# Performance work log

Measured on AMD Instinct MI355X. Metric: run time of the kernel, lower is better.

Reference implementation:

```python
import math
import jax, jax.numpy as jnp
import numpy as np

LMAX = 6
SH_DIM = (LMAX + 1) ** 2
NUM_INV = LMAX + 1
SILU_SCALE = 1.0 / 0.6  # ScaledSiLU


def scaled_silu(x):
    return jax.nn.silu(x) * SILU_SCALE


def sph_harm(v):
    """Real spherical harmonics up to LMAX, 'component' normalization, input normalized. [*, 3] -> [*, SH_DIM]."""
    n = jnp.sqrt(jnp.sum(v * v, axis=-1, keepdims=True) + 1e-12)
    v = v / n
    x, y, z = v[..., 0], v[..., 1], v[..., 2]
    st = jnp.sqrt(jnp.clip(x * x + y * y, 0.0, None))  # sin(theta)
    phi = jnp.arctan2(y, x)
    # fully-normalized associated Legendre P[(l,m)] via standard recurrences
    P = {(0, 0): jnp.full_like(z, math.sqrt(1.0 / (4.0 * math.pi)))}
    for m in range(1, LMAX + 1):
        P[(m, m)] = -math.sqrt((2 * m + 1) / (2.0 * m)) * st * P[(m - 1, m - 1)]
    for m in range(0, LMAX):
        P[(m + 1, m)] = math.sqrt(2 * m + 3) * z * P[(m, m)]
    for m in range(0, LMAX + 1):
        for l in range(m + 2, LMAX + 1):
            a = math.sqrt((4 * l * l - 1.0) / (l * l - m * m))
            b = math.sqrt(((l - 1) ** 2 - m * m) / (4.0 * (l - 1) ** 2 - 1.0))
            P[(l, m)] = a * (z * P[(l - 1, m)] - b * P[(l - 2, m)])
    s4pi = math.sqrt(4.0 * math.pi)
    sq2 = math.sqrt(2.0)
    cols = []
    for l in range(LMAX + 1):
        for m in range(-l, l + 1):
            if m < 0:
                cols.append(s4pi * sq2 * P[(l, -m)] * jnp.sin(-m * phi))
            elif m == 0:
                cols.append(s4pi * P[(l, 0)])
            else:
                cols.append(s4pi * sq2 * P[(l, m)] * jnp.cos(m * phi))
    return jnp.stack(cols, axis=-1)


def sh_bilinear_inv(sh1, sh2):
    """Per-l mean of elementwise product. [E, SH_DIM] x2 -> [E, NUM_INV]."""
    outs, idx = [], 0
    for l in range(LMAX + 1):
        d = 2 * l + 1
        outs.append(jnp.mean(sh1[:, idx:idx + d] * sh2[:, idx:idx + d], axis=-1))
        idx += d
    return jnp.stack(outs, axis=-1)


def _forward(node_scalar, node_vector, edge_rbf, edge_udiff, edge_index,
             W_edge, b_edge, W_x1, b_x1, W_x2, b_x2, ln_g, ln_b, W_inv, b_inv):
    H = node_scalar.shape[1]
    N = node_scalar.shape[0]
    j, i = edge_index[0], edge_index[1]
    inv_sqrt3 = 1.0 / math.sqrt(3.0)
    inv_sqrt_h = 1.0 / math.sqrt(H)

    rbf_h = edge_rbf @ W_edge + b_edge  # [E, 3H]

    # scatter-mean of edge directions onto receiving nodes
    counts = jax.ops.segment_sum(jnp.ones_like(i, dtype=edge_udiff.dtype), i, num_segments=N)
    ref_vec = jax.ops.segment_sum(edge_udiff, i, num_segments=N) / jnp.maximum(counts, 1.0)[:, None]
    ref_norm = jnp.sqrt(jnp.sum(ref_vec * ref_vec, axis=-1, keepdims=True) + 1e-9)
    ref_vec = ref_vec / ref_norm
    zero_mask = ref_norm[:, 0] < 5e-5
    default_vec = jnp.array([1.0, 0.0, 0.0], dtype=ref_vec.dtype)
    ref_vec = jnp.where(zero_mask[:, None], default_vec, ref_vec)

    edge_sh = sph_harm(edge_udiff)          # [E, SH_DIM]
    ref_sh = sph_harm(ref_vec)[i]           # [E, SH_DIM]
    inv = sh_bilinear_inv(edge_sh, ref_sh)  # [E, NUM_INV]
    mu = jnp.mean(inv, axis=-1, keepdims=True)
    var = jnp.var(inv, axis=-1, keepdims=True)
    inv = (inv - mu) / jnp.sqrt(var + 1e-5) * ln_g + ln_b

    cos_theta = jnp.sum(edge_udiff * ref_vec[i], axis=-1, keepdims=True)  # [E,1]
    geom = jnp.concatenate([cos_theta, inv], axis=-1)  # [E, NUM_INV+1]
    gate = jnp.tanh(scaled_silu(geom @ W_inv + b_inv))
    rbf_h = rbf_h * (1.0 + gate)

    scalar_proj = scaled_silu(node_scalar @ W_x1 + b_x1) @ W_x2 + b_x2  # [N, 3H]
    x_ji = scalar_proj[j] * rbf_h * inv_sqrt3
    x1, x2, x3 = x_ji[:, :H], x_ji[:, H:2 * H], x_ji[:, 2 * H:]

    vec_ji = (x1[:, None, :] * node_vector[j] + x2[:, None, :] * edge_udiff[:, :, None]) * inv_sqrt_h  # [E,3,H]
    delta_vector = jax.ops.segment_sum(vec_ji, i, num_segments=N)
    delta_scalar = jax.ops.segment_sum(x3, i, num_segments=N)
    return delta_scalar, delta_vector


def setup_inputs() -> dict:
    N, E, H, R = 50000, 400000, 64, 64
    key = jax.random.key(0)
    ks = jax.random.split(key, 16)
    ud = jax.random.normal(ks[3], (E, 3), dtype=jnp.float32)
    ud = ud / jnp.linalg.norm(ud, axis=-1, keepdims=True)
    s = 0.05
    return {
        "node_scalar": jax.random.normal(ks[0], (N, H), dtype=jnp.float32),
        "node_vector": jax.random.normal(ks[1], (N, 3, H), dtype=jnp.float32),
        "edge_rbf": jax.random.uniform(ks[2], (E, R), dtype=jnp.float32),
        "edge_udiff": ud,
        "edge_index": jax.random.randint(ks[4], (2, E), 0, N, dtype=jnp.int32),
        "W_edge": jax.random.normal(ks[5], (R, 3 * H), dtype=jnp.float32) * s,
        "b_edge": jnp.zeros((3 * H,), dtype=jnp.float32),
        "W_x1": jax.random.normal(ks[6], (H, H // 2), dtype=jnp.float32) * s,
        "b_x1": jnp.zeros((H // 2,), dtype=jnp.float32),
        "W_x2": jax.random.normal(ks[7], (H // 2, 3 * H), dtype=jnp.float32) * s,
        "b_x2": jnp.zeros((3 * H,), dtype=jnp.float32),
        "ln_g": jnp.ones((NUM_INV,), dtype=jnp.float32),
        "ln_b": jnp.zeros((NUM_INV,), dtype=jnp.float32),
        "W_inv": jax.random.normal(ks[8], (NUM_INV + 1, 3 * H), dtype=jnp.float32) * s,
        "b_inv": jnp.zeros((3 * H,), dtype=jnp.float32),
    }


def reference(node_scalar, node_vector, edge_rbf, edge_udiff, edge_index,
              W_edge, b_edge, W_x1, b_x1, W_x2, b_x2, ln_g, ln_b, W_inv, b_inv):
    return _forward(node_scalar, node_vector, edge_rbf, edge_udiff, edge_index,
                    W_edge, b_edge, W_x1, b_x1, W_x2, b_x2, ln_g, ln_b, W_inv, b_inv)
```

## Files before the change

### kernel.cpp

```cpp
#include <hip/hip_runtime.h>
#include <math.h>

#define LMAXX 6
#define SH49 49
#define TPB 256
#define TILE_E 64
#define SCB 256
#define CAPS 14

typedef __attribute__((ext_vector_type(8))) short short8v;
typedef __attribute__((ext_vector_type(16))) float f32x16;
union FragU { short8v v; uint2 u2[2]; };

__device__ __forceinline__ unsigned pack_bf16(float a, float b) {
    unsigned ua = __float_as_uint(a);
    unsigned ub = __float_as_uint(b);
    ua += 0x7fffu + ((ua >> 16) & 1u);
    ub += 0x7fffu + ((ub >> 16) & 1u);
    return (ua >> 16) | (ub & 0xffff0000u);
}
__device__ __forceinline__ float bf16_lo(unsigned w) { return __uint_as_float(w << 16); }
__device__ __forceinline__ float bf16_hi(unsigned w) { return __uint_as_float(w & 0xffff0000u); }

__device__ __forceinline__ void sph49(float x, float y, float z, float* sh) {
    float nn = sqrtf(x * x + y * y + z * z + 1e-12f);
    float iv = 1.0f / nn;
    x *= iv; y *= iv; z *= iv;
    float st2 = x * x + y * y;
    float st = sqrtf(st2 > 0.f ? st2 : 0.f);
    float cphi, sphi;
    if (st > 1e-30f) { cphi = x / st; sphi = y / st; }
    else { cphi = 1.0f; sphi = 0.0f; }

    float P[LMAXX + 1][LMAXX + 1];
    P[0][0] = 0.28209479177387814f;
#pragma unroll
    for (int m = 1; m <= LMAXX; ++m)
        P[m][m] = -sqrtf((2.f * m + 1.f) / (2.f * m)) * st * P[m - 1][m - 1];
#pragma unroll
    for (int m = 0; m < LMAXX; ++m)
        P[m + 1][m] = sqrtf(2.f * m + 3.f) * z * P[m][m];
#pragma unroll
    for (int m = 0; m <= LMAXX; ++m) {
#pragma unroll
        for (int l = m + 2; l <= LMAXX; ++l) {
            float a = sqrtf((4.f * l * l - 1.f) / (float)(l * l - m * m));
            float b = sqrtf((float)((l - 1) * (l - 1) - m * m) /
                            (4.f * (l - 1) * (l - 1) - 1.f));
            P[l][m] = a * (z * P[l - 1][m] - b * P[l - 2][m]);
        }
    }
    float cm[LMAXX + 1], sm[LMAXX + 1];
    cm[0] = 1.f; sm[0] = 0.f; cm[1] = cphi; sm[1] = sphi;
#pragma unroll
    for (int m = 2; m <= LMAXX; ++m) {
        cm[m] = 2.f * cphi * cm[m - 1] - cm[m - 2];
        sm[m] = 2.f * cphi * sm[m - 1] - sm[m - 2];
    }
    const float s4pi = 3.5449077018110318f;
    const float s8pi = 5.0132565492620005f;
    int idx = 0;
#pragma unroll
    for (int l = 0; l <= LMAXX; ++l) {
#pragma unroll
        for (int mm = -l; mm <= l; ++mm) {
            if (mm < 0)       sh[idx++] = s8pi * P[l][-mm] * sm[-mm];
            else if (mm == 0) sh[idx++] = s4pi * P[l][0];
            else              sh[idx++] = s8pi * P[l][mm] * cm[mm];
        }
    }
}

__global__ void k_hist(const int* __restrict__ eidx, int* __restrict__ icnt, int E) {
    int e = blockIdx.x * blockDim.x + threadIdx.x;
    if (e >= E) return;
    atomicAdd(&icnt[eidx[E + e]], 1);
}

__global__ void k_scan1(const int* __restrict__ icnt, int* __restrict__ offs,
                        int* __restrict__ bsum, int N) {
    __shared__ int s[SCB];
    int t = threadIdx.x;
    int idx = blockIdx.x * SCB + t;
    int v = (idx < N) ? icnt[idx] : 0;
    s[t] = v; __syncthreads();
#pragma unroll
    for (int off = 1; off < SCB; off <<= 1) {
        int u = (t >= off) ? s[t - off] : 0;
        __syncthreads();
        s[t] += u;
        __syncthreads();
    }
    if (idx < N) offs[idx] = s[t] - v;
    if (t == SCB - 1) bsum[blockIdx.x] = s[t];
}

__global__ void k_scan2(int* __restrict__ bsum, int nb) {
    __shared__ int s[1024];
    int t = threadIdx.x;
    int v = (t < nb) ? bsum[t] : 0;
    s[t] = v; __syncthreads();
#pragma unroll
    for (int off = 1; off < 1024; off <<= 1) {
        int u = (t >= off) ? s[t - off] : 0;
        __syncthreads();
        s[t] += u;
        __syncthreads();
    }
    if (t < nb) bsum[t] = s[t] - v;
}

__global__ void k_scan3(int* __restrict__ offs, const int* __restrict__ bsum,
                        int* __restrict__ cursor, int N) {
    int idx = blockIdx.x * SCB + threadIdx.x;
    if (idx >= N) return;
    int o = offs[idx] + bsum[blockIdx.x];
    offs[idx] = o;
    cursor[idx] = o;
}

__global__ void k_perm(const float* __restrict__ ud, const int* __restrict__ eidx,
                       int* __restrict__ cursor, int* __restrict__ perm,
                       int* __restrict__ ii_s, int* __restrict__ jj_s,
                       float* __restrict__ ud_s, int E) {
    int e = blockIdx.x * blockDim.x + threadIdx.x;
    if (e >= E) return;
    int i = eidx[E + e];
    int j = eidx[e];
    int pos = atomicAdd(&cursor[i], 1);
    perm[pos] = e;
    ii_s[pos] = i;
    jj_s[pos] = j;
    ud_s[3 * pos + 0] = ud[3 * e + 0];
    ud_s[3 * pos + 1] = ud[3 * e + 1];
    ud_s[3 * pos + 2] = ud[3 * e + 2];
}

__global__ void k_node_ref(const int* __restrict__ offs, const int* __restrict__ icnt,
                           const float* __restrict__ ud_s,
                           float* __restrict__ ref_vec, float* __restrict__ ref_sh,
                           int N) {
    int n = blockIdx.x * blockDim.x + threadIdx.x;
    if (n >= N) return;
    int o0 = offs[n], c = icnt[n];
    float sx = 0.f, sy = 0.f, sz = 0.f;
    for (int e = o0; e < o0 + c; ++e) {
        sx += ud_s[3 * e + 0];
        sy += ud_s[3 * e + 1];
        sz += ud_s[3 * e + 2];
    }
    float d = fmaxf((float)c, 1.0f);
    float vx = sx / d, vy = sy / d, vz = sz / d;
    float norm = sqrtf(vx * vx + vy * vy + vz * vz + 1e-9f);
    float ivn = 1.0f / norm;
    vx *= ivn; vy *= ivn; vz *= ivn;
    if (norm < 5e-5f) { vx = 1.f; vy = 0.f; vz = 0.f; }
    ref_vec[3 * n + 0] = vx;
    ref_vec[3 * n + 1] = vy;
    ref_vec[3 * n + 2] = vz;
    sph49(vx, vy, vz, ref_sh + (size_t)n * SH49);
}

__global__ __launch_bounds__(TPB) void k_sproj(const float* __restrict__ ns,
                                               const float* __restrict__ W1,
                                               const float* __restrict__ b1,
                                               const float* __restrict__ W2,
                                               const float* __restrict__ b2,
                                               unsigned* __restrict__ spj_p, int N) {
    __shared__ float sW1[64 * 32];
    __shared__ float sW2[32 * 192];
    __shared__ float sb2[192];
    __shared__ float sb1[32];
    __shared__ float sbuf[4][64];
    __shared__ float h1buf[4][32];
    __shared__ float srow[4][192];
    int t = threadIdx.x;
    for (int p = t; p < 64 * 32; p += TPB) sW1[p] = W1[p];
    for (int p = t; p < 32 * 192; p += TPB) sW2[p] = W2[p];
    if (t < 192) sb2[t] = b2[t];
    if (t < 32) sb1[t] = b1[t];

    int w = t >> 6, l = t & 63;
    int nwaves = gridDim.x * 4;
    int iters = (N + nwaves - 1) / nwaves;
    for (int it = 0; it < iters; ++it) {
        int n = blockIdx.x * 4 + w + it * nwaves;
        bool act = n < N;
        __syncthreads();
        if (act) sbuf[w][l] = ns[(size_t)n * 64 + l];
        __syncthreads();
        if (act) {
            int k = l & 31;
            float h = sb1[k];
#pragma unroll
            for (int c = 0; c < 64; ++c) h = fmaf(sbuf[w][c], sW1[c * 32 + k], h);
            float sig = 1.0f / (1.0f + __expf(-h));
            h = h * sig * (1.0f / 0.6f);
            if (l < 32) h1buf[w][l] = h;
        }
        __syncthreads();
        if (act) {
#pragma unroll
            for (int m = 0; m < 3; ++m) {
                int o = l + 64 * m;
                float a = sb2[o];
#pragma unroll
                for (int kk = 0; kk < 32; ++kk)
                    a = fmaf(h1buf[w][kk], sW2[kk * 192 + o], a);
                srow[w][o] = a;
            }
        }
        __syncthreads();
        if (act) {
            {
                int ww = l;
                if (ww < 96) {
                    int oc = ww & 31, q = ww >> 5;
                    spj_p[(size_t)n * 96 + ww] =
                        pack_bf16(srow[w][64 * q + oc], srow[w][64 * q + oc + 32]);
                }
            }
            if (l < 32) {
                int ww = 64 + l;
                int oc = ww & 31, q = ww >> 5;
                spj_p[(size_t)n * 96 + ww] =
                    pack_bf16(srow[w][64 * q + oc], srow[w][64 * q + oc + 32]);
            }
        }
    }
}

__global__ void k_nvp(const float* __restrict__ nvec, unsigned* __restrict__ nvp,
                      int total ) {
    int idx = blockIdx.x * blockDim.x + threadIdx.x;
    if (idx >= total) return;
    int n = idx / 96, w = idx - n * 96;
    int d = w >> 5, oc = w & 31;
    size_t base = (size_t)n * 192 + d * 64 + oc;
    nvp[idx] = pack_bf16(nvec[base], nvec[base + 32]);
}

__global__ void k_geom_s(const float* __restrict__ ud_s, const int* __restrict__ ii_s,
                         const float* __restrict__ ref_vec,
                         const float* __restrict__ ref_sh,
                         const float* __restrict__ ln_g, const float* __restrict__ ln_b,
                         float* __restrict__ geom_s, int E) {
    int r = blockIdx.x * blockDim.x + threadIdx.x;
    if (r >= E) return;
    int i = ii_s[r];
    float ux = ud_s[3 * r], uy = ud_s[3 * r + 1], uz = ud_s[3 * r + 2];
    float esh[SH49];
    sph49(ux, uy, uz, esh);
    const float* rs = ref_sh + (size_t)i * SH49;
    float inv[7];
    int idx = 0;
#pragma unroll
    for (int l = 0; l <= 6; ++l) {
        float s = 0.f;
#pragma unroll
        for (int m = 0; m < 2 * l + 1; ++m) { s += esh[idx] * rs[idx]; idx++; }
        inv[l] = s / (float)(2 * l + 1);
    }
    float mu = 0.f;
#pragma unroll
    for (int l = 0; l < 7; ++l) mu += inv[l];
    mu *= (1.0f / 7.0f);
    float var = 0.f;
#pragma unroll
    for (int l = 0; l < 7; ++l) { float d = inv[l] - mu; var += d * d; }
    var *= (1.0f / 7.0f);
    float rstd = rsqrtf(var + 1e-5f);
    float rvx = ref_vec[3 * i], rvy = ref_vec[3 * i + 1], rvz = ref_vec[3 * i + 2];
    float ct = ux * rvx + uy * rvy + uz * rvz;
    float* g = geom_s + (size_t)r * 8;
    g[0] = ct;
#pragma unroll
    for (int l = 0; l < 7; ++l) g[1 + l] = (inv[l] - mu) * rstd * ln_g[l] + ln_b[l];
}

__global__ __launch_bounds__(TPB, 3) void k_main(
    const float* __restrict__ rbf, const float* __restrict__ W_edge,
    const float* __restrict__ b_edge, const float* __restrict__ W_inv,
    const float* __restrict__ b_inv, const float* __restrict__ geom_s,
    const unsigned* __restrict__ spj_p, const unsigned* __restrict__ nvp,
    const float* __restrict__ ud_s, const int* __restrict__ ii_s,
    const int* __restrict__ jj_s, const int* __restrict__ perm,
    float* __restrict__ dscal, float* __restrict__ dvec, int E) {
    __shared__ __align__(16) unsigned sWT[192 * 34];
    __shared__ __align__(16) unsigned rbfT[64 * 34];
    __shared__ __align__(16) float sgeom[64 * 8];
    __shared__ float sud[64 * 3];
    __shared__ int sii[64];
    __shared__ int sjj[64];
    __shared__ int sslot[64];
    __shared__ int sfirst[64];
    __shared__ int sD;
    __shared__ float sacc[CAPS * 256];

    int t = threadIdx.x;
    int l = t & 63;
    int wid = t >> 6;
    int eh = wid >> 1;
    int wc = wid & 1;
    int lo5 = l & 31;
    int hi = l >> 5;
    int h = wc * 32 + lo5;

    for (int p = t; p < 192 * 32; p += TPB) {
        int col = p >> 5, kd = p & 31;
        sWT[col * 34 + kd] = pack_bf16(W_edge[(2 * kd) * 192 + col],
                                       W_edge[(2 * kd + 1) * 192 + col]);
    }

    float wv_inv[8][3];
#pragma unroll
    for (int c = 0; c < 8; ++c)
#pragma unroll
        for (int q = 0; q < 3; ++q)
            wv_inv[c][q] = W_inv[c * 192 + q * 64 + h];
    float bi[3], be[3];
#pragma unroll
    for (int q = 0; q < 3; ++q) {
        bi[q] = b_inv[q * 64 + h];
        be[q] = b_edge[q * 64 + h];
    }

    const float inv_sqrt3 = 0.57735026918962584f;
    const float inv_sqrt_h = 0.125f;

    int ntiles = (E + TILE_E - 1) / TILE_E;
    for (int tile = blockIdx.x; tile < ntiles; tile += gridDim.x) {
        int e0 = tile * TILE_E;
        __syncthreads();
        if (t < 64) {
            int rg = e0 + t;
            sjj[t] = (rg < E) ? jj_s[rg] : 0;
            sii[t] = (rg < E) ? ii_s[rg] : -1;
        }
        for (int p = t; p < 64 * 8; p += TPB)
            sgeom[p] = (e0 + (p >> 3) < E) ? geom_s[(size_t)e0 * 8 + p] : 0.f;
        for (int p = t; p < 64 * 3; p += TPB)
            sud[p] = (e0 + p / 3 < E) ? ud_s[(size_t)e0 * 3 + p] : 0.f;
        {
            int e = t >> 2, q4 = t & 3;
            int rg = e0 + e;
            int dst = e * 34 + q4 * 8;
            if (rg < E) {
                const float4* src = (const float4*)&rbf[(size_t)perm[rg] * 64 + q4 * 16];
                float4 v0 = src[0], v1 = src[1], v2 = src[2], v3 = src[3];
                rbfT[dst + 0] = pack_bf16(v0.x, v0.y);
                rbfT[dst + 1] = pack_bf16(v0.z, v0.w);
                rbfT[dst + 2] = pack_bf16(v1.x, v1.y);
                rbfT[dst + 3] = pack_bf16(v1.z, v1.w);
                rbfT[dst + 4] = pack_bf16(v2.x, v2.y);
                rbfT[dst + 5] = pack_bf16(v2.z, v2.w);
                rbfT[dst + 6] = pack_bf16(v3.x, v3.y);
                rbfT[dst + 7] = pack_bf16(v3.z, v3.w);
            } else {
#pragma unroll
                for (int q = 0; q < 8; ++q) rbfT[dst + q] = 0u;
            }
        }
        __syncthreads();

        if (t < 64) {
            bool flag = (t == 0) || (sii[t] != sii[t - 1]);
            unsigned long long bal = __ballot(flag);
            unsigned long long mask =
                (t == 63) ? ~0ull : ((1ull << (t + 1)) - 1ull);
            int slot = __popcll(bal & mask) - 1;
            sslot[t] = slot;
            if (flag) sfirst[slot] = t;
            if (t == 0) sD = __popcll(bal);
        }

        FragU afr[4];
        int arow = lo5 + 32 * eh;
#pragma unroll
        for (int ks = 0; ks < 4; ++ks) {
            int off = arow * 34 + ks * 8 + hi * 4;
            afr[ks].u2[0] = *(const uint2*)&rbfT[off];
            afr[ks].u2[1] = *(const uint2*)&rbfT[off + 2];
        }
        f32x16 acc0 = {0.f,0.f,0.f,0.f,0.f,0.f,0.f,0.f,0.f,0.f,0.f,0.f,0.f,0.f,0.f,0.f};
        f32x16 acc1 = acc0, acc2 = acc0;
        int bc0 = (wc * 32 + lo5) * 34;
#pragma unroll
        for (int ks = 0; ks < 4; ++ks) {
            int off = ks * 8 + hi * 4;
            FragU b0, b1, b2;
            b0.u2[0] = *(const uint2*)&sWT[bc0 + off];
            b0.u2[1] = *(const uint2*)&sWT[bc0 + off + 2];
            b1.u2[0] = *(const uint2*)&sWT[bc0 + 64 * 34 + off];
            b1.u2[1] = *(const uint2*)&sWT[bc0 + 64 * 34 + off + 2];
            b2.u2[0] = *(const uint2*)&sWT[bc0 + 128 * 34 + off];
            b2.u2[1] = *(const uint2*)&sWT[bc0 + 128 * 34 + off + 2];
            acc0 = __builtin_amdgcn_mfma_f32_32x32x16_bf16(afr[ks].v, b0.v, acc0, 0, 0, 0);
            acc1 = __builtin_amdgcn_mfma_f32_32x32x16_bf16(afr[ks].v, b1.v, acc1, 0, 0, 0);
            acc2 = __builtin_amdgcn_mfma_f32_32x32x16_bf16(afr[ks].v, b2.v, acc2, 0, 0, 0);
        }

        __syncthreads();
        int D = sD;
        bool slotmode = (D <= CAPS);
        if (slotmode) {
            for (int p = t; p < D * 256; p += TPB) sacc[p] = 0.f;
        }
        __syncthreads();

        float a_s = 0.f, a_v0 = 0.f, a_v1 = 0.f, a_v2 = 0.f;
        int runi = -1, runslot = -1;
        auto flush = [&]() {
            if (runi < 0) return;
            if (slotmode) {
                float* sa = &sacc[runslot * 256];
                atomicAdd(&sa[h], a_s);
                atomicAdd(&sa[64 + h], a_v0);
                atomicAdd(&sa[128 + h], a_v1);
                atomicAdd(&sa[192 + h], a_v2);
            } else {
                atomicAdd(&dscal[(size_t)runi * 64 + h], a_s);
                atomicAdd(&dvec[(size_t)runi * 192 + h], a_v0);
                atomicAdd(&dvec[(size_t)runi * 192 + 64 + h], a_v1);
                atomicAdd(&dvec[(size_t)runi * 192 + 128 + h], a_v2);
            }
        };
#pragma unroll
        for (int r = 0; r < 16; ++r) {
            int el = eh * 32 + (r & 3) + 8 * (r >> 2) + 4 * hi;
            int rg = e0 + el;
            if (rg < E) {
                int i = sii[el], j = sjj[el];
                if (i != runi) {
                    flush();
                    a_s = 0.f; a_v0 = 0.f; a_v1 = 0.f; a_v2 = 0.f;
                    runi = i; runslot = sslot[el];
                }
                float4 g0 = *(const float4*)&sgeom[el * 8];
                float4 g1 = *(const float4*)&sgeom[el * 8 + 4];
                float u0 = bi[0], u1 = bi[1], u2 = bi[2];
                float gg[8] = {g0.x, g0.y, g0.z, g0.w, g1.x, g1.y, g1.z, g1.w};
#pragma unroll
                for (int c = 0; c < 8; ++c) {
                    u0 = fmaf(gg[c], wv_inv[c][0], u0);
                    u1 = fmaf(gg[c], wv_inv[c][1], u1);
                    u2 = fmaf(gg[c], wv_inv[c][2], u2);
                }
                float gate[3];
                float uu[3] = {u0, u1, u2};
#pragma unroll
                for (int q = 0; q < 3; ++q) {
                    float u = uu[q];
                    float sig = 1.0f / (1.0f + __expf(-u));
                    float v = u * sig * (1.0f / 0.6f);
                    v = fminf(fmaxf(v, -20.f), 20.f);
                    float e2v = __expf(2.0f * v);
                    gate[q] = (e2v - 1.0f) / (e2v + 1.0f);
                }
                size_t jb = (size_t)j * 96;
                unsigned spw0 = spj_p[jb + lo5];
                unsigned spw1 = spj_p[jb + 32 + lo5];
                unsigned spw2 = spj_p[jb + 64 + lo5];
                float sp0 = wc ? bf16_hi(spw0) : bf16_lo(spw0);
                float sp1 = wc ? bf16_hi(spw1) : bf16_lo(spw1);
                float sp2 = wc ? bf16_hi(spw2) : bf16_lo(spw2);
                float x1 = sp0 * (acc0[r] + be[0]) * (1.0f + gate[0]) * inv_sqrt3;
                float x2 = sp1 * (acc1[r] + be[1]) * (1.0f + gate[1]) * inv_sqrt3;
                float x3 = sp2 * (acc2[r] + be[2]) * (1.0f + gate[2]) * inv_sqrt3;
                a_s += x3;
                float ud0 = sud[el * 3], ud1 = sud[el * 3 + 1], ud2 = sud[el * 3 + 2];
                unsigned nw0 = nvp[jb + lo5];
                unsigned nw1 = nvp[jb + 32 + lo5];
                unsigned nw2 = nvp[jb + 64 + lo5];
                float nv0 = wc ? bf16_hi(nw0) : bf16_lo(nw0);
                float nv1 = wc ? bf16_hi(nw1) : bf16_lo(nw1);
                float nv2 = wc ? bf16_hi(nw2) : bf16_lo(nw2);
                a_v0 += (x1 * nv0 + x2 * ud0) * inv_sqrt_h;
                a_v1 += (x1 * nv1 + x2 * ud1) * inv_sqrt_h;
                a_v2 += (x1 * nv2 + x2 * ud2) * inv_sqrt_h;
            }
        }
        flush();
        __syncthreads();

        if (slotmode) {
            int Dreal = D - ((sii[63] < 0) ? 1 : 0);
            for (int s = 0; s < D; ++s) {
                int n = sii[sfirst[s]];
                if (n < 0) continue;
                float val = sacc[s * 256 + t];
                bool boundary = (s == 0) || (s == Dreal - 1);
                float* ptr = (t < 64) ? &dscal[(size_t)n * 64 + t]
                                      : &dvec[(size_t)n * 192 + (t - 64)];
                if (boundary) atomicAdd(ptr, val);
                else *ptr = val;
            }
        }
    }
}

extern "C" void kernel_launch(void* const* d_in, const int* in_sizes, int n_in,
                              void* d_out, int out_size, void* d_ws, size_t ws_size,
                              hipStream_t stream) {
    const float* node_scalar = (const float*)d_in[0];
    const float* node_vector = (const float*)d_in[1];
    const float* edge_rbf    = (const float*)d_in[2];
    const float* edge_udiff  = (const float*)d_in[3];
    const int*   edge_index  = (const int*)d_in[4];
    const float* W_edge      = (const float*)d_in[5];
    const float* b_edge      = (const float*)d_in[6];
    const float* W_x1        = (const float*)d_in[7];
    const float* b_x1        = (const float*)d_in[8];
    const float* W_x2        = (const float*)d_in[9];
    const float* b_x2        = (const float*)d_in[10];
    const float* ln_g        = (const float*)d_in[11];
    const float* ln_b        = (const float*)d_in[12];
    const float* W_inv       = (const float*)d_in[13];
    const float* b_inv       = (const float*)d_in[14];

    int N = in_sizes[0] / 64;
    int E = in_sizes[3] / 3;

    float* ws = (float*)d_ws;
    size_t o = 0;
    int*      icnt   = (int*)(ws + o); o += N;
    int*      offs   = (int*)(ws + o); o += N;
    int*      cursor = (int*)(ws + o); o += N;
    int*      bsum   = (int*)(ws + o); o += 1024;
    float*    ref_vec= ws + o; o += (size_t)N * 3;
    float*    ref_sh = ws + o; o += (size_t)N * SH49;
    unsigned* spj_p  = (unsigned*)(ws + o); o += (size_t)N * 96;
    unsigned* nvp    = (unsigned*)(ws + o); o += (size_t)N * 96;
    int*      perm   = (int*)(ws + o); o += E;
    float*    geom_s = ws + o; o += (size_t)E * 8;
    float*    ud_s   = ws + o; o += (size_t)E * 3;
    int*      ii_s   = (int*)(ws + o); o += E;
    int*      jj_s   = (int*)(ws + o); o += E;

    float* dscal = (float*)d_out;
    float* dvec  = (float*)d_out + (size_t)N * 64;

    hipMemsetAsync(icnt, 0, (size_t)N * sizeof(int), stream);
    hipMemsetAsync(d_out, 0, (size_t)out_size * sizeof(float), stream);

    int nb = (N + SCB - 1) / SCB;

    k_hist<<<(E + TPB - 1) / TPB, TPB, 0, stream>>>(edge_index, icnt, E);
    k_scan1<<<nb, SCB, 0, stream>>>(icnt, offs, bsum, N);
    k_scan2<<<1, 1024, 0, stream>>>(bsum, nb);
    k_scan3<<<nb, SCB, 0, stream>>>(offs, bsum, cursor, N);
    k_perm<<<(E + TPB - 1) / TPB, TPB, 0, stream>>>(edge_udiff, edge_index, cursor,
                                                    perm, ii_s, jj_s, ud_s, E);
    k_node_ref<<<(N + TPB - 1) / TPB, TPB, 0, stream>>>(offs, icnt, ud_s,
                                                        ref_vec, ref_sh, N);
    k_sproj<<<512, TPB, 0, stream>>>(node_scalar, W_x1, b_x1, W_x2, b_x2, spj_p, N);
    k_nvp<<<(N * 96 + TPB - 1) / TPB, TPB, 0, stream>>>(node_vector, nvp, N * 96);
    k_geom_s<<<(E + TPB - 1) / TPB, TPB, 0, stream>>>(ud_s, ii_s, ref_vec, ref_sh,
                                                      ln_g, ln_b, geom_s, E);
    k_main<<<768, TPB, 0, stream>>>(edge_rbf, W_edge, b_edge, W_inv, b_inv, geom_s,
                                    spj_p, nvp, ud_s, ii_s, jj_s, perm,
                                    dscal, dvec, E);
}
```

Measured before the change: 632.4 us.

## Fuse node gather buffers, compute SH invariant via Legendre product, drop LDS staging

Result: faster. 576.2 us (-8.9%).

```diff
diff --git a/kernel.cpp b/kernel.cpp
--- a/kernel.cpp
+++ b/kernel.cpp
@@ -2,11 +2,10 @@
 #include <math.h>
 
 #define LMAXX 6
-#define SH49 49
 #define TPB 256
 #define TILE_E 64
 #define SCB 256
-#define CAPS 14
+#define CAPS 12
 
 typedef __attribute__((ext_vector_type(8))) short short8v;
 typedef __attribute__((ext_vector_type(16))) float f32x16;
@@ -22,17 +21,18 @@
 __device__ __forceinline__ float bf16_lo(unsigned w) { return __uint_as_float(w << 16); }
 __device__ __forceinline__ float bf16_hi(unsigned w) { return __uint_as_float(w & 0xffff0000u); }
 
-__device__ __forceinline__ void sph49(float x, float y, float z, float* sh) {
+__device__ __forceinline__ void dirang(float x, float y, float z,
+                                       float& zo, float& st, float& cphi, float& sphi) {
     float nn = sqrtf(x * x + y * y + z * z + 1e-12f);
     float iv = 1.0f / nn;
-    x *= iv; y *= iv; z *= iv;
+    x *= iv; y *= iv; zo = z * iv;
     float st2 = x * x + y * y;
-    float st = sqrtf(st2 > 0.f ? st2 : 0.f);
-    float cphi, sphi;
+    st = sqrtf(st2 > 0.f ? st2 : 0.f);
     if (st > 1e-30f) { cphi = x / st; sphi = y / st; }
     else { cphi = 1.0f; sphi = 0.0f; }
-
-    float P[LMAXX + 1][LMAXX + 1];
+}
+
+__device__ __forceinline__ void legP(float z, float st, float P[7][7]) {
     P[0][0] = 0.28209479177387814f;
 #pragma unroll
     for (int m = 1; m <= LMAXX; ++m)
@@ -48,25 +48,6 @@
             float b = sqrtf((float)((l - 1) * (l - 1) - m * m) /
                             (4.f * (l - 1) * (l - 1) - 1.f));
             P[l][m] = a * (z * P[l - 1][m] - b * P[l - 2][m]);
-        }
-    }
-    float cm[LMAXX + 1], sm[LMAXX + 1];
-    cm[0] = 1.f; sm[0] = 0.f; cm[1] = cphi; sm[1] = sphi;
-#pragma unroll
-    for (int m = 2; m <= LMAXX; ++m) {
-        cm[m] = 2.f * cphi * cm[m - 1] - cm[m - 2];
-        sm[m] = 2.f * cphi * sm[m - 1] - sm[m - 2];
-    }
-    const float s4pi = 3.5449077018110318f;
-    const float s8pi = 5.0132565492620005f;
-    int idx = 0;
-#pragma unroll
-    for (int l = 0; l <= LMAXX; ++l) {
-#pragma unroll
-        for (int mm = -l; mm <= l; ++mm) {
-            if (mm < 0)       sh[idx++] = s8pi * P[l][-mm] * sm[-mm];
-            else if (mm == 0) sh[idx++] = s4pi * P[l][0];
-            else              sh[idx++] = s8pi * P[l][mm] * cm[mm];
         }
     }
 }
@@ -138,8 +119,7 @@
 
 __global__ void k_node_ref(const int* __restrict__ offs, const int* __restrict__ icnt,
                            const float* __restrict__ ud_s,
-                           float* __restrict__ ref_vec, float* __restrict__ ref_sh,
-                           int N) {
+                           float* __restrict__ ref_vec, int N) {
     int n = blockIdx.x * blockDim.x + threadIdx.x;
     if (n >= N) return;
     int o0 = offs[n], c = icnt[n];
@@ -158,22 +138,21 @@
     ref_vec[3 * n + 0] = vx;
     ref_vec[3 * n + 1] = vy;
     ref_vec[3 * n + 2] = vz;
-    sph49(vx, vy, vz, ref_sh + (size_t)n * SH49);
-}
-
-__global__ __launch_bounds__(TPB) void k_sproj(const float* __restrict__ ns,
-                                               const float* __restrict__ W1,
-                                               const float* __restrict__ b1,
-                                               const float* __restrict__ W2,
-                                               const float* __restrict__ b2,
-                                               unsigned* __restrict__ spj_p, int N) {
+}
+
+__global__ __launch_bounds__(TPB) void k_sprojv(const float* __restrict__ ns,
+                                                const float* __restrict__ W1,
+                                                const float* __restrict__ b1,
+                                                const float* __restrict__ W2,
+                                                const float* __restrict__ b2,
+                                                const float* __restrict__ nvec,
+                                                unsigned* __restrict__ gat, int N) {
     __shared__ float sW1[64 * 32];
     __shared__ float sW2[32 * 192];
     __shared__ float sb2[192];
     __shared__ float sb1[32];
     __shared__ float sbuf[4][64];
     __shared__ float h1buf[4][32];
-    __shared__ float srow[4][192];
     int t = threadIdx.x;
     for (int p = t; p < 64 * 32; p += TPB) sW1[p] = W1[p];
     for (int p = t; p < 32 * 192; p += TPB) sW2[p] = W2[p];
@@ -200,67 +179,70 @@
         }
         __syncthreads();
         if (act) {
+            float a[3];
 #pragma unroll
             for (int m = 0; m < 3; ++m) {
                 int o = l + 64 * m;
-                float a = sb2[o];
+                float acc = sb2[o];
 #pragma unroll
                 for (int kk = 0; kk < 32; ++kk)
-                    a = fmaf(h1buf[w][kk], sW2[kk * 192 + o], a);
-                srow[w][o] = a;
+                    acc = fmaf(h1buf[w][kk], sW2[kk * 192 + o], acc);
+                a[m] = acc;
             }
-        }
-        __syncthreads();
-        if (act) {
-            {
-                int ww = l;
-                if (ww < 96) {
-                    int oc = ww & 31, q = ww >> 5;
-                    spj_p[(size_t)n * 96 + ww] =
-                        pack_bf16(srow[w][64 * q + oc], srow[w][64 * q + oc + 32]);
-                }
-            }
-            if (l < 32) {
-                int ww = 64 + l;
-                int oc = ww & 31, q = ww >> 5;
-                spj_p[(size_t)n * 96 + ww] =
-                    pack_bf16(srow[w][64 * q + oc], srow[w][64 * q + oc + 32]);
-            }
-        }
-    }
-}
-
-__global__ void k_nvp(const float* __restrict__ nvec, unsigned* __restrict__ nvp,
-                      int total ) {
-    int idx = blockIdx.x * blockDim.x + threadIdx.x;
-    if (idx >= total) return;
-    int n = idx / 96, w = idx - n * 96;
-    int d = w >> 5, oc = w & 31;
-    size_t base = (size_t)n * 192 + d * 64 + oc;
-    nvp[idx] = pack_bf16(nvec[base], nvec[base + 32]);
+            size_t nb = (size_t)n * 192;
+            float nv0 = nvec[nb + l];
+            float nv1 = nvec[nb + 64 + l];
+            float nv2 = nvec[nb + 128 + l];
+            gat[nb + l]        = pack_bf16(a[0], a[1]);
+            gat[nb + 64 + l]   = pack_bf16(a[2], nv0);
+            gat[nb + 128 + l]  = pack_bf16(nv1, nv2);
+        }
+    }
 }
 
 __global__ void k_geom_s(const float* __restrict__ ud_s, const int* __restrict__ ii_s,
                          const float* __restrict__ ref_vec,
-                         const float* __restrict__ ref_sh,
                          const float* __restrict__ ln_g, const float* __restrict__ ln_b,
                          float* __restrict__ geom_s, int E) {
     int r = blockIdx.x * blockDim.x + threadIdx.x;
     if (r >= E) return;
     int i = ii_s[r];
     float ux = ud_s[3 * r], uy = ud_s[3 * r + 1], uz = ud_s[3 * r + 2];
-    float esh[SH49];
-    sph49(ux, uy, uz, esh);
-    const float* rs = ref_sh + (size_t)i * SH49;
+    float rvx = ref_vec[3 * i], rvy = ref_vec[3 * i + 1], rvz = ref_vec[3 * i + 2];
+
+    float zE, stE, cpE, spE, zR, stR, cpR, spR;
+    dirang(ux, uy, uz, zE, stE, cpE, spE);
+    dirang(rvx, rvy, rvz, zR, stR, cpR, spR);
+
+    float Pe[7][7], Pr[7][7];
+    legP(zE, stE, Pe);
+    legP(zR, stR, Pr);
+
+    float cmE[7], smE[7], cmR[7], smR[7];
+    cmE[0] = 1.f; smE[0] = 0.f; cmE[1] = cpE; smE[1] = spE;
+    cmR[0] = 1.f; smR[0] = 0.f; cmR[1] = cpR; smR[1] = spR;
+#pragma unroll
+    for (int m = 2; m <= LMAXX; ++m) {
+        cmE[m] = 2.f * cpE * cmE[m - 1] - cmE[m - 2];
+        smE[m] = 2.f * cpE * smE[m - 1] - smE[m - 2];
+        cmR[m] = 2.f * cpR * cmR[m - 1] - cmR[m - 2];
+        smR[m] = 2.f * cpR * smR[m - 1] - smR[m - 2];
+    }
+
     float inv[7];
-    int idx = 0;
-#pragma unroll
-    for (int l = 0; l <= 6; ++l) {
-        float s = 0.f;
-#pragma unroll
-        for (int m = 0; m < 2 * l + 1; ++m) { s += esh[idx] * rs[idx]; idx++; }
-        inv[l] = s / (float)(2 * l + 1);
-    }
+#pragma unroll
+    for (int l = 0; l <= LMAXX; ++l) inv[l] = Pe[l][0] * Pr[l][0];
+#pragma unroll
+    for (int m = 1; m <= LMAXX; ++m) {
+        float cross = cmE[m] * cmR[m] + smE[m] * smR[m];
+#pragma unroll
+        for (int l = m; l <= LMAXX; ++l)
+            inv[l] += 2.f * Pe[l][m] * Pr[l][m] * cross;
+    }
+    const float fourpi = 12.566370614359172f;
+#pragma unroll
+    for (int l = 0; l <= LMAXX; ++l) inv[l] *= fourpi / (float)(2 * l + 1);
+
     float mu = 0.f;
 #pragma unroll
     for (int l = 0; l < 7; ++l) mu += inv[l];
@@ -270,7 +252,6 @@
     for (int l = 0; l < 7; ++l) { float d = inv[l] - mu; var += d * d; }
     var *= (1.0f / 7.0f);
     float rstd = rsqrtf(var + 1e-5f);
-    float rvx = ref_vec[3 * i], rvy = ref_vec[3 * i + 1], rvz = ref_vec[3 * i + 2];
     float ct = ux * rvx + uy * rvy + uz * rvz;
     float* g = geom_s + (size_t)r * 8;
     g[0] = ct;
@@ -278,20 +259,16 @@
     for (int l = 0; l < 7; ++l) g[1 + l] = (inv[l] - mu) * rstd * ln_g[l] + ln_b[l];
 }
 
-__global__ __launch_bounds__(TPB, 3) void k_main(
+__global__ __launch_bounds__(TPB, 4) void k_main(
     const float* __restrict__ rbf, const float* __restrict__ W_edge,
     const float* __restrict__ b_edge, const float* __restrict__ W_inv,
     const float* __restrict__ b_inv, const float* __restrict__ geom_s,
-    const unsigned* __restrict__ spj_p, const unsigned* __restrict__ nvp,
-    const float* __restrict__ ud_s, const int* __restrict__ ii_s,
-    const int* __restrict__ jj_s, const int* __restrict__ perm,
+    const unsigned* __restrict__ gat, const float* __restrict__ ud_s,
+    const int* __restrict__ ii_s, const int* __restrict__ jj_s,
+    const int* __restrict__ perm,
     float* __restrict__ dscal, float* __restrict__ dvec, int E) {
     __shared__ __align__(16) unsigned sWT[192 * 34];
-    __shared__ __align__(16) unsigned rbfT[64 * 34];
-    __shared__ __align__(16) float sgeom[64 * 8];
-    __shared__ float sud[64 * 3];
     __shared__ int sii[64];
-    __shared__ int sjj[64];
     __shared__ int sslot[64];
     __shared__ int sfirst[64];
     __shared__ int sD;
@@ -334,32 +311,7 @@
         __syncthreads();
         if (t < 64) {
             int rg = e0 + t;
-            sjj[t] = (rg < E) ? jj_s[rg] : 0;
             sii[t] = (rg < E) ? ii_s[rg] : -1;
-        }
-        for (int p = t; p < 64 * 8; p += TPB)
-            sgeom[p] = (e0 + (p >> 3) < E) ? geom_s[(size_t)e0 * 8 + p] : 0.f;
-        for (int p = t; p < 64 * 3; p += TPB)
-            sud[p] = (e0 + p / 3 < E) ? ud_s[(size_t)e0 * 3 + p] : 0.f;
-        {
-            int e = t >> 2, q4 = t & 3;
-            int rg = e0 + e;
-            int dst = e * 34 + q4 * 8;
-            if (rg < E) {
-                const float4* src = (const float4*)&rbf[(size_t)perm[rg] * 64 + q4 * 16];
-                float4 v0 = src[0], v1 = src[1], v2 = src[2], v3 = src[3];
-                rbfT[dst + 0] = pack_bf16(v0.x, v0.y);
-                rbfT[dst + 1] = pack_bf16(v0.z, v0.w);
-                rbfT[dst + 2] = pack_bf16(v1.x, v1.y);
-                rbfT[dst + 3] = pack_bf16(v1.z, v1.w);
-                rbfT[dst + 4] = pack_bf16(v2.x, v2.y);
-                rbfT[dst + 5] = pack_bf16(v2.z, v2.w);
-                rbfT[dst + 6] = pack_bf16(v3.x, v3.y);
-                rbfT[dst + 7] = pack_bf16(v3.z, v3.w);
-            } else {
-#pragma unroll
-                for (int q = 0; q < 8; ++q) rbfT[dst + q] = 0u;
-            }
         }
         __syncthreads();
 
@@ -376,12 +328,25 @@
 
         FragU afr[4];
         int arow = lo5 + 32 * eh;
-#pragma unroll
-        for (int ks = 0; ks < 4; ++ks) {
-            int off = arow * 34 + ks * 8 + hi * 4;
-            afr[ks].u2[0] = *(const uint2*)&rbfT[off];
-            afr[ks].u2[1] = *(const uint2*)&rbfT[off + 2];
-        }
+        int rga = e0 + arow;
+        if (rga < E) {
+            int row = perm[rga];
+            const float4* rp = (const float4*)&rbf[(size_t)row * 64 + hi * 8];
+#pragma unroll
+            for (int ks = 0; ks < 4; ++ks) {
+                float4 f0 = rp[ks * 4];
+                float4 f1 = rp[ks * 4 + 1];
+                afr[ks].u2[0] = make_uint2(pack_bf16(f0.x, f0.y), pack_bf16(f0.z, f0.w));
+                afr[ks].u2[1] = make_uint2(pack_bf16(f1.x, f1.y), pack_bf16(f1.z, f1.w));
+            }
+        } else {
+#pragma unroll
+            for (int ks = 0; ks < 4; ++ks) {
+                afr[ks].u2[0] = make_uint2(0u, 0u);
+                afr[ks].u2[1] = make_uint2(0u, 0u);
+            }
+        }
+
         f32x16 acc0 = {0.f,0.f,0.f,0.f,0.f,0.f,0.f,0.f,0.f,0.f,0.f,0.f,0.f,0.f,0.f,0.f};
         f32x16 acc1 = acc0, acc2 = acc0;
         int bc0 = (wc * 32 + lo5) * 34;
@@ -430,14 +395,16 @@
             int el = eh * 32 + (r & 3) + 8 * (r >> 2) + 4 * hi;
             int rg = e0 + el;
             if (rg < E) {
-                int i = sii[el], j = sjj[el];
+                int i = sii[el];
+                int j = jj_s[rg];
                 if (i != runi) {
                     flush();
                     a_s = 0.f; a_v0 = 0.f; a_v1 = 0.f; a_v2 = 0.f;
                     runi = i; runslot = sslot[el];
                 }
-                float4 g0 = *(const float4*)&sgeom[el * 8];
-                float4 g1 = *(const float4*)&sgeom[el * 8 + 4];
+                const float4* gp = (const float4*)(geom_s + (size_t)rg * 8);
+                float4 g0 = gp[0];
+                float4 g1 = gp[1];
                 float u0 = bi[0], u1 = bi[1], u2 = bi[2];
                 float gg[8] = {g0.x, g0.y, g0.z, g0.w, g1.x, g1.y, g1.z, g1.w};
 #pragma unroll
@@ -457,24 +424,19 @@
                     float e2v = __expf(2.0f * v);
                     gate[q] = (e2v - 1.0f) / (e2v + 1.0f);
                 }
-                size_t jb = (size_t)j * 96;
-                unsigned spw0 = spj_p[jb + lo5];
-                unsigned spw1 = spj_p[jb + 32 + lo5];
-                unsigned spw2 = spj_p[jb + 64 + lo5];
-                float sp0 = wc ? bf16_hi(spw0) : bf16_lo(spw0);
-                float sp1 = wc ? bf16_hi(spw1) : bf16_lo(spw1);
-                float sp2 = wc ? bf16_hi(spw2) : bf16_lo(spw2);
+                size_t jb = (size_t)j * 192;
+                unsigned w0 = gat[jb + h];
+                unsigned w1 = gat[jb + 64 + h];
+                unsigned w2 = gat[jb + 128 + h];
+                float sp0 = bf16_lo(w0), sp1 = bf16_hi(w0), sp2 = bf16_lo(w1);
+                float nv0 = bf16_hi(w1), nv1 = bf16_lo(w2), nv2 = bf16_hi(w2);
                 float x1 = sp0 * (acc0[r] + be[0]) * (1.0f + gate[0]) * inv_sqrt3;
                 float x2 = sp1 * (acc1[r] + be[1]) * (1.0f + gate[1]) * inv_sqrt3;
                 float x3 = sp2 * (acc2[r] + be[2]) * (1.0f + gate[2]) * inv_sqrt3;
                 a_s += x3;
-                float ud0 = sud[el * 3], ud1 = sud[el * 3 + 1], ud2 = sud[el * 3 + 2];
-                unsigned nw0 = nvp[jb + lo5];
-                unsigned nw1 = nvp[jb + 32 + lo5];
-                unsigned nw2 = nvp[jb + 64 + lo5];
-                float nv0 = wc ? bf16_hi(nw0) : bf16_lo(nw0);
-                float nv1 = wc ? bf16_hi(nw1) : bf16_lo(nw1);
-                float nv2 = wc ? bf16_hi(nw2) : bf16_lo(nw2);
+                float ud0 = ud_s[3 * rg + 0];
+                float ud1 = ud_s[3 * rg + 1];
+                float ud2 = ud_s[3 * rg + 2];
                 a_v0 += (x1 * nv0 + x2 * ud0) * inv_sqrt_h;
                 a_v1 += (x1 * nv1 + x2 * ud1) * inv_sqrt_h;
                 a_v2 += (x1 * nv2 + x2 * ud2) * inv_sqrt_h;
@@ -523,19 +485,18 @@
 
     float* ws = (float*)d_ws;
     size_t o = 0;
-    int*      icnt   = (int*)(ws + o); o += N;
-    int*      offs   = (int*)(ws + o); o += N;
-    int*      cursor = (int*)(ws + o); o += N;
-    int*      bsum   = (int*)(ws + o); o += 1024;
-    float*    ref_vec= ws + o; o += (size_t)N * 3;
-    float*    ref_sh = ws + o; o += (size_t)N * SH49;
-    unsigned* spj_p  = (unsigned*)(ws + o); o += (size_t)N * 96;
-    unsigned* nvp    = (unsigned*)(ws + o); o += (size_t)N * 96;
-    int*      perm   = (int*)(ws + o); o += E;
-    float*    geom_s = ws + o; o += (size_t)E * 8;
-    float*    ud_s   = ws + o; o += (size_t)E * 3;
-    int*      ii_s   = (int*)(ws + o); o += E;
-    int*      jj_s   = (int*)(ws + o); o += E;
+    auto A4 = [&]() { o = (o + 3) & ~(size_t)3; };
+    int*      icnt   = (int*)(ws + o); o += N; A4();
+    int*      offs   = (int*)(ws + o); o += N; A4();
+    int*      cursor = (int*)(ws + o); o += N; A4();
+    int*      bsum   = (int*)(ws + o); o += 1024; A4();
+    float*    ref_vec= ws + o; o += (size_t)N * 3; A4();
+    unsigned* gat    = (unsigned*)(ws + o); o += (size_t)N * 192; A4();
+    int*      perm   = (int*)(ws + o); o += E; A4();
+    float*    geom_s = ws + o; o += (size_t)E * 8; A4();
+    float*    ud_s   = ws + o; o += (size_t)E * 3; A4();
+    int*      ii_s   = (int*)(ws + o); o += E; A4();
+    int*      jj_s   = (int*)(ws + o); o += E; A4();
 
     float* dscal = (float*)d_out;
     float* dvec  = (float*)d_out + (size_t)N * 64;
@@ -551,13 +512,11 @@
     k_scan3<<<nb, SCB, 0, stream>>>(offs, bsum, cursor, N);
     k_perm<<<(E + TPB - 1) / TPB, TPB, 0, stream>>>(edge_udiff, edge_index, cursor,
                                                     perm, ii_s, jj_s, ud_s, E);
-    k_node_ref<<<(N + TPB - 1) / TPB, TPB, 0, stream>>>(offs, icnt, ud_s,
-                                                        ref_vec, ref_sh, N);
-    k_sproj<<<512, TPB, 0, stream>>>(node_scalar, W_x1, b_x1, W_x2, b_x2, spj_p, N);
-    k_nvp<<<(N * 96 + TPB - 1) / TPB, TPB, 0, stream>>>(node_vector, nvp, N * 96);
-    k_geom_s<<<(E + TPB - 1) / TPB, TPB, 0, stream>>>(ud_s, ii_s, ref_vec, ref_sh,
+    k_node_ref<<<(N + TPB - 1) / TPB, TPB, 0, stream>>>(offs, icnt, ud_s, ref_vec, N);
+    k_sprojv<<<512, TPB, 0, stream>>>(node_scalar, W_x1, b_x1, W_x2, b_x2,
+                                      node_vector, gat, N);
+    k_geom_s<<<(E + TPB - 1) / TPB, TPB, 0, stream>>>(ud_s, ii_s, ref_vec,
                                                       ln_g, ln_b, geom_s, E);
-    k_main<<<768, TPB, 0, stream>>>(edge_rbf, W_edge, b_edge, W_inv, b_inv, geom_s,
-                                    spj_p, nvp, ud_s, ii_s, jj_s, perm,
-                                    dscal, dvec, E);
-}
+    k_main<<<1024, TPB, 0, stream>>>(edge_rbf, W_edge, b_edge, W_inv, b_inv, geom_s,
+                                     gat, ud_s, ii_s, jj_s, perm, dscal, dvec, E);
+}
```
